# Optimization experiments

Hardware: AMD Instinct MI355X
Metric: run time of the kernel (lower is better)

Reference implementation:

```python
import math
import jax, jax.numpy as jnp
import numpy as np

MUL = 8      # multiplicity of 0e and 1o in irreps_in/out
KS = 5       # kernel spatial extent (diameter 5, steps 1 -> coords -2..2)
NB = 5       # num_radial_basis
RAD = 2.5    # diameter / 2


def _sus(t):
    # e3nn sus(x) = exp(-1/x) for x>0 else 0
    return jnp.where(t > 0.0, jnp.exp(-1.0 / jnp.where(t > 0.0, t, 1.0)), 0.0)


def _emb_sh():
    c = jnp.arange(-2.0, 3.0)
    lat = jnp.stack(jnp.meshgrid(c, c, c, indexing='ij'), axis=-1)  # (5,5,5,3)
    d = jnp.linalg.norm(lat, axis=-1)
    # soft_one_hot_linspace(basis='smooth_finite', cutoff=True)
    values = jnp.linspace(0.0, RAD, NB + 2)
    step = values[1] - values[0]
    diff = (d[..., None] - values[1:-1]) / step
    emb = 1.14136 * math.exp(2.0) * _sus(diff + 1.0) * _sus(1.0 - diff)  # (5,5,5,NB)
    # real spherical harmonics, lmax=2, normalize=True, normalization='component'
    safe = jnp.where(d > 0.0, d, 1.0)[..., None]
    u = jnp.where(d[..., None] > 0.0, lat / safe, 0.0)
    x, y, z = u[..., 0], u[..., 1], u[..., 2]
    s3, s5, s15 = math.sqrt(3.0), math.sqrt(5.0), math.sqrt(15.0)
    sh = jnp.stack([
        jnp.ones_like(x),
        s3 * x, s3 * y, s3 * z,
        s15 * x * z, s15 * x * y,
        s5 * (y * y - 0.5 * (x * x + z * z)),
        s15 * y * z, (s15 / 2.0) * (z * z - x * x),
    ], axis=-1)  # (5,5,5,9)
    return emb, sh


def _c121():
    # Clebsch-Gordan (w3j) for 1o x 2e -> 1o in the real e3nn basis, built from the
    # orthonormal symmetric-traceless matrix basis matching the l=2 SH component order.
    s2, s6 = math.sqrt(2.0), math.sqrt(6.0)
    S = np.zeros((5, 3, 3))
    S[0, 0, 2] = S[0, 2, 0] = 1.0 / s2            # xz
    S[1, 0, 1] = S[1, 1, 0] = 1.0 / s2            # xy
    S[2] = np.diag([-1.0, 2.0, -1.0]) / s6        # 2y^2 - x^2 - z^2
    S[3, 1, 2] = S[3, 2, 1] = 1.0 / s2            # yz
    S[4] = np.diag([-1.0, 0.0, 1.0]) / s2         # z^2 - x^2
    # w3j(1,2,1)[m,j,k] = S[j,m,k]/sqrt(5)  (fully symmetric since l1+l2+l3 even)
    return jnp.asarray(np.transpose(S, (1, 0, 2)) / math.sqrt(5.0), dtype=jnp.float32)


def _build_kernel(weight, emb, sh, c121, dtype):
    g = (KS, KS, KS)
    W = (emb @ weight) / float(KS * KS * KS)  # (5,5,5,320)
    w1, w2, w3, w4, w5 = [W[..., 64 * i:64 * (i + 1)].reshape(g + (MUL, MUL)) for i in range(5)]
    sh0, sh1, sh2 = sh[..., 0], sh[..., 1:4], sh[..., 4:9]
    pw0 = math.sqrt(1.0 / 16.0)   # output 0e: alpha=1, fan_in=8+8
    pw1 = math.sqrt(3.0 / 24.0)   # output 1o: alpha=3, fan_in=8+8+8
    inv_s3 = 1.0 / math.sqrt(3.0)
    K00 = pw0 * sh0[..., None, None] * w1                                   # (g,u,w)
    K01 = (pw1 * inv_s3) * jnp.einsum('xyzuw,xyzk->xyzuwk', w2, sh1)        # (g,u,w,k)
    K10 = (pw0 * inv_s3) * jnp.einsum('xyzuw,xyzm->xyzumw', w4, sh1)        # (g,u,m,w)
    T = jnp.einsum('xyzj,mjk->xyzmk', sh2, c121)                            # (g,m,k)
    eye3 = jnp.eye(3, dtype=dtype)
    K11 = pw1 * (inv_s3 * jnp.einsum('xyzuw,mk->xyzumwk', sh0[..., None, None] * w3, eye3)
                 + jnp.einsum('xyzuw,xyzmk->xyzumwk', w5, T))               # (g,u,m,w,k)
    D = 4 * MUL
    kern = jnp.zeros(g + (D, D), dtype=dtype)
    kern = kern.at[..., :MUL, :MUL].set(K00)
    kern = kern.at[..., :MUL, MUL:].set(K01.reshape(g + (MUL, 3 * MUL)))
    kern = kern.at[..., MUL:, :MUL].set(K10.reshape(g + (3 * MUL, MUL)))
    kern = kern.at[..., MUL:, MUL:].set(K11.reshape(g + (3 * MUL, 3 * MUL)))
    return jnp.transpose(kern, (4, 3, 0, 1, 2))  # 'xyzio->oixyz'


def reference(x, weight, w_sc0, w_sc1):
    emb, sh = _emb_sh()
    c121 = _c121()
    kern = _build_kernel(weight, emb, sh, c121, x.dtype)
    B, _, X, Y, Z = x.shape
    inv_s8 = 1.0 / math.sqrt(MUL)
    # self-connection: e3nn Linear, 0e->0e and 1o->1o blocks
    x0 = x[:, :MUL]
    x1 = x[:, MUL:].reshape(B, MUL, 3, X, Y, Z)
    sc0 = inv_s8 * jnp.einsum('uv,buxyz->bvxyz', w_sc0, x0)
    sc1 = inv_s8 * jnp.einsum('uv,bumxyz->bvmxyz', w_sc1, x1).reshape(B, 3 * MUL, X, Y, Z)
    sc = jnp.concatenate([sc0, sc1], axis=1)
    conv = jax.lax.conv_general_dilated(
        x, kern, window_strides=(1, 1, 1), padding=[(2, 2)] * 3,
        dimension_numbers=('NCDHW', 'OIDHW', 'NCDHW'))
    return sc + conv


def setup_inputs() -> dict:
    key = jax.random.key(0)
    k1, k2, k3, k4 = jax.random.split(key, 4)
    return {
        'x': jax.random.normal(k1, (2, 32, 64, 64, 64), dtype=jnp.float32),
        'weight': jax.random.normal(k2, (NB, 5 * MUL * MUL), dtype=jnp.float32),
        'w_sc0': jax.random.normal(k3, (MUL, MUL), dtype=jnp.float32),
        'w_sc1': jax.random.normal(k4, (MUL, MUL), dtype=jnp.float32),
    }
```

## Files before the change

### kernel.cpp

```cpp
#include <hip/hip_runtime.h>
#include <math.h>

typedef __attribute__((ext_vector_type(8))) short short8;
typedef __attribute__((ext_vector_type(4))) float f32x4;
typedef __attribute__((ext_vector_type(16))) float f32x16;

#define NTAP 125
#define DCH 32

static __device__ __forceinline__ unsigned short f2bf(float f) {
    union { float f; unsigned u; } v; v.f = f;
    unsigned u = v.u;
    return (unsigned short)((u + 0x7FFFu + ((u >> 16) & 1u)) >> 16);
}

static __device__ __forceinline__ void gld_lds16(const void* g, void* l) {
    __builtin_amdgcn_global_load_lds(
        (const __attribute__((address_space(1))) unsigned int*)g,
        (__attribute__((address_space(3))) unsigned int*)l, 16, 0, 0);
}

__global__ __launch_bounds__(128) void build_kern(
    const float* __restrict__ weight,
    const float* __restrict__ w_sc0,
    const float* __restrict__ w_sc1,
    float* __restrict__ kw)
{
    const int t = blockIdx.x;
    const int dx = t / 25, dy = (t / 5) % 5, dz = t % 5;
    const float px = dx - 2.0f, py = dy - 2.0f, pz = dz - 2.0f;
    const float d = sqrtf(px * px + py * py + pz * pz);

    const float stepv = 2.5f / 6.0f;
    const float embc = 1.14136f * expf(2.0f);
    float emb[5];
#pragma unroll
    for (int n = 0; n < 5; ++n) {
        float diff = (d - stepv * (float)(n + 1)) / stepv;
        float a = diff + 1.0f, bb = 1.0f - diff;
        float v = 0.0f;
        if (a > 0.0f && bb > 0.0f)
            v = embc * expf(-1.0f / a) * expf(-1.0f / bb);
        emb[n] = v;
    }

    const float inv_d = (d > 0.0f) ? 1.0f / d : 0.0f;
    const float ux = px * inv_d, uy = py * inv_d, uz = pz * inv_d;
    const float s3 = 1.73205081f, s5 = 2.23606798f, s15 = 3.87298335f;
    float sh[9];
    sh[0] = 1.0f;
    sh[1] = s3 * ux; sh[2] = s3 * uy; sh[3] = s3 * uz;
    sh[4] = s15 * ux * uz;
    sh[5] = s15 * ux * uy;
    sh[6] = s5 * (uy * uy - 0.5f * (ux * ux + uz * uz));
    sh[7] = s15 * uy * uz;
    sh[8] = 0.5f * s15 * (uz * uz - ux * ux);

    const float i_s2 = 0.70710678f, i_s6 = 0.40824829f, i_s5 = 0.44721360f;
    float T[3][3];
    T[0][0] = i_s5 * (-sh[6] * i_s6 - sh[8] * i_s2);
    T[0][1] = i_s5 * (sh[5] * i_s2);
    T[0][2] = i_s5 * (sh[4] * i_s2);
    T[1][0] = T[0][1];
    T[1][1] = i_s5 * (2.0f * sh[6] * i_s6);
    T[1][2] = i_s5 * (sh[7] * i_s2);
    T[2][0] = T[0][2];
    T[2][1] = T[1][2];
    T[2][2] = i_s5 * (-sh[6] * i_s6 + sh[8] * i_s2);

    __shared__ float Wt[320];
    for (int col = threadIdx.x; col < 320; col += 128) {
        float a = 0.0f;
#pragma unroll
        for (int n = 0; n < 5; ++n) a += emb[n] * weight[n * 320 + col];
        Wt[col] = a * (1.0f / 125.0f);
    }
    __syncthreads();

    const float pw0 = 0.25f;
    const float pw1 = 0.35355339f;
    const float inv_s3 = 0.57735027f;
    const float inv_s8 = 0.35355339f;

    for (int idx = threadIdx.x; idx < 1024; idx += 128) {
        const int o = idx >> 5, i = idx & 31;
        float val;
        if (o < 8) {
            if (i < 8) {
                val = pw0 * Wt[i * 8 + o];
            } else {
                const int u = (i - 8) / 3, m = (i - 8) % 3;
                val = pw0 * inv_s3 * Wt[192 + u * 8 + o] * sh[1 + m];
            }
        } else {
            const int v = (o - 8) / 3, k = (o - 8) % 3;
            if (i < 8) {
                val = pw1 * inv_s3 * Wt[64 + i * 8 + v] * sh[1 + k];
            } else {
                const int u = (i - 8) / 3, m = (i - 8) % 3;
                float tv = Wt[256 + u * 8 + v] * T[m][k];
                if (m == k) tv += inv_s3 * Wt[128 + u * 8 + v];
                val = pw1 * tv;
            }
        }
        if (t == 62) {
            if (o < 8 && i < 8) {
                val += inv_s8 * w_sc0[i * 8 + o];
            } else if (o >= 8 && i >= 8) {
                const int u = (i - 8) / 3, m = (i - 8) % 3;
                const int v = (o - 8) / 3, k = (o - 8) % 3;
                if (m == k) val += inv_s8 * w_sc1[u * 8 + v];
            }
        }
        kw[(i * NTAP + t) * DCH + o] = val;
    }
}

__global__ __launch_bounds__(128) void pack_b(
    const float* __restrict__ kw, unsigned short* __restrict__ kwb)
{
    const int t = blockIdx.x;
    const int tid = threadIdx.x;
    const int kh = tid >> 6, l = tid & 63;
    const int co = l & 31;
    const int cib = kh * 16 + (l >> 5) * 8;
    unsigned short v[8];
#pragma unroll
    for (int j = 0; j < 8; ++j)
        v[j] = f2bf(kw[((cib + j) * NTAP + t) * DCH + co]);
    uint4 o;
    o.x = (unsigned)v[0] | ((unsigned)v[1] << 16);
    o.y = (unsigned)v[2] | ((unsigned)v[3] << 16);
    o.z = (unsigned)v[4] | ((unsigned)v[5] << 16);
    o.w = (unsigned)v[6] | ((unsigned)v[7] << 16);
    *reinterpret_cast<uint4*>(kwb + ((size_t)(t * 2 + kh) * 64 + l) * 8) = o;
}

__global__ __launch_bounds__(256) void xpose(
    const float* __restrict__ x, unsigned short* __restrict__ xt)
{
    const int xx = blockIdx.x, yy = blockIdx.y, b = blockIdx.z;
    const int t = threadIdx.x;
    const int z = t & 63, part = t >> 6;
    const float* src = x + ((((size_t)b * 32) * 64 + xx) * 64 + yy) * 64 + z;
    unsigned short v[8];
#pragma unroll
    for (int j = 0; j < 8; ++j)
        v[j] = f2bf(src[(size_t)(part * 8 + j) * 262144]);
    uint4 o;
    o.x = (unsigned)v[0] | ((unsigned)v[1] << 16);
    o.y = (unsigned)v[2] | ((unsigned)v[3] << 16);
    o.z = (unsigned)v[4] | ((unsigned)v[5] << 16);
    o.w = (unsigned)v[6] | ((unsigned)v[7] << 16);
    *reinterpret_cast<uint4*>(
        xt + ((((size_t)b * 64 + xx) * 64 + yy) * 64 + z) * 32 + part * 8) = o;
}

__global__ void zero_fill(float4* p) {
    p[threadIdx.x] = make_float4(0.f, 0.f, 0.f, 0.f);
}

__global__ __launch_bounds__(256, 2) void conv_mfma(
    const unsigned short* __restrict__ xt,
    const unsigned short* __restrict__ kwb,
    const unsigned short* __restrict__ zpage,
    float* __restrict__ out)
{
    extern __shared__ unsigned short smem[];
    char* lds = (char*)smem;

    const int tid = threadIdx.x;
    const int lane = tid & 63;
    const int wv = tid >> 6;
    const int oyp = wv >> 1, zh = wv & 1;
    const int x0 = blockIdx.x * 4, y0 = blockIdx.y * 4;
    const int b = blockIdx.z;
    const int l31 = lane & 31, hi = lane >> 5;

    int abase[5][2];
#pragma unroll
    for (int dz = 0; dz < 5; ++dz) {
        const int s = zh * 32 + l31 + dz;
#pragma unroll
        for (int kh = 0; kh < 2; ++kh) {
            const int cph = (kh * 2 + hi) ^ ((s >> 1) & 3);
            abase[dz][kh] = 51200 + (((((oyp * 2) * 68 + s) << 2) | cph) << 4);
        }
    }
    const int bbase = lane * 16;

    int srow[5]; int soff[5]; bool szok[5];
#pragma unroll
    for (int p = 0; p < 5; ++p) {
        const int c = tid + p * 256;
        const int row = c / 272;
        const int rem = c - row * 272;
        const int slot = rem >> 2;
        const int clog = (rem & 3) ^ ((slot >> 1) & 3);
        const int z = slot - 2;
        srow[p] = row;
        szok[p] = ((unsigned)z < 64u);
        soff[p] = row * 2048 + z * 32 + clog * 8;
    }

    int bsrc[13];
#pragma unroll
    for (int k = 0; k < 13; ++k) {
        const int c = tid + k * 256;
        const int tp = c >> 7, rem = c & 127;
        const int dxx = tp / 5, dzz = tp - dxx * 5;
        bsrc[k] = (dxx * 25 + dzz) * 128 + rem;
    }

    f32x16 acc[2][4];
#pragma unroll
    for (int oyi = 0; oyi < 2; ++oyi)
#pragma unroll
        for (int ox = 0; ox < 4; ++ox)
#pragma unroll
            for (int e = 0; e < 16; ++e) acc[oyi][ox][e] = 0.0f;

    for (int dy = 0; dy < 5; ++dy) {
        const int yyb = y0 + dy - 2;
#pragma unroll
        for (int xl = 0; xl < 8; ++xl) {
            __syncthreads();
            if (xl == 0) {
#pragma unroll
                for (int k = 0; k < 13; ++k) {
                    const int c0 = wv * 64 + k * 256;
                    if (c0 < 3200) {
                        gld_lds16(kwb + ((size_t)(bsrc[k] + dy * 640)) * 8,
                                  lds + c0 * 16);
                    }
                }
            }
            {
                const int xx = x0 + xl - 2;
                const bool xok = ((unsigned)xx < 64u);
                const long long xyb =
                    (long long)(b * 64 + xx) * 131072 + (long long)yyb * 2048;
#pragma unroll
                for (int p = 0; p < 5; ++p) {
                    const int c0 = wv * 64 + p * 256;
                    if (c0 < 1088) {
                        const int yy = yyb + srow[p];
                        const bool ok =
                            xok && ((unsigned)yy < 64u) && szok[p];
                        const unsigned short* src =
                            ok ? (xt + xyb + soff[p]) : zpage;
                        gld_lds16(src, lds + 51200 + c0 * 16);
                    }
                }
            }
            __syncthreads();

#pragma unroll
            for (int dz = 0; dz < 5; ++dz) {
#pragma unroll
                for (int kh = 0; kh < 2; ++kh) {
                    const short8 a0 =
                        *reinterpret_cast<const short8*>(lds + abase[dz][kh]);
                    const short8 a1 = *reinterpret_cast<const short8*>(
                        lds + abase[dz][kh] + 4352);
#pragma unroll
                    for (int ox = 0; ox < 4; ++ox) {
                        const int dxv = xl - ox;
                        if (dxv < 0 || dxv > 4) continue;
                        const short8 bf = *reinterpret_cast<const short8*>(
                            lds + bbase + (((dxv * 5 + dz) * 2 + kh) << 10));
                        acc[0][ox] = __builtin_amdgcn_mfma_f32_32x32x16_bf16(
                            a0, bf, acc[0][ox], 0, 0, 0);
                        acc[1][ox] = __builtin_amdgcn_mfma_f32_32x32x16_bf16(
                            a1, bf, acc[1][ox], 0, 0, 0);
                    }
                }
            }
        }
    }

#pragma unroll
    for (int oyi = 0; oyi < 2; ++oyi) {
        const int yy = y0 + oyp * 2 + oyi;
#pragma unroll
        for (int ox = 0; ox < 4; ++ox) {
            float* base = out +
                ((((size_t)b * 32 + l31) * 64 + (x0 + ox)) * 64 + yy) * 64 +
                zh * 32 + hi * 4;
#pragma unroll
            for (int rq = 0; rq < 4; ++rq) {
                f32x4 v = { acc[oyi][ox][rq * 4 + 0], acc[oyi][ox][rq * 4 + 1],
                            acc[oyi][ox][rq * 4 + 2], acc[oyi][ox][rq * 4 + 3] };
                *reinterpret_cast<f32x4*>(base + rq * 8) = v;
            }
        }
    }
}

extern "C" void kernel_launch(void* const* d_in, const int* in_sizes, int n_in,
                              void* d_out, int out_size, void* d_ws, size_t ws_size,
                              hipStream_t stream) {
    const float* x      = (const float*)d_in[0];
    const float* weight = (const float*)d_in[1];
    const float* w_sc0  = (const float*)d_in[2];
    const float* w_sc1  = (const float*)d_in[3];
    float* out = (float*)d_out;

    char* ws = (char*)d_ws;
    unsigned short* xt  = (unsigned short*)ws;
    float*          kwp = (float*)(ws + 33554432);
    unsigned short* kwb = (unsigned short*)(ws + 34066432);
    unsigned short* zpg = (unsigned short*)(ws + 34322432);

    (void)hipFuncSetAttribute((const void*)conv_mfma,
                              hipFuncAttributeMaxDynamicSharedMemorySize,
                              68608);

    hipLaunchKernelGGL(build_kern, dim3(NTAP), dim3(128), 0, stream,
                       weight, w_sc0, w_sc1, kwp);
    hipLaunchKernelGGL(pack_b, dim3(NTAP), dim3(128), 0, stream, kwp, kwb);
    hipLaunchKernelGGL(xpose, dim3(64, 64, 2), dim3(256), 0, stream, x, xt);
    hipLaunchKernelGGL(zero_fill, dim3(1), dim3(256), 0, stream, (float4*)zpg);
    hipLaunchKernelGGL(conv_mfma, dim3(16, 16, 2), dim3(256), 68608, stream,
                       xt, kwb, zpg, out);
}
```

Baseline: 152.9 us.

## Prefetch next input slab into registers to overlap global loads with MFMA

Input-slab loads move from direct global-to-LDS transfers issued just before use to register prefetches issued one iteration ahead. The data is then written to LDS at the top of the next iteration. Plain __syncthreads is replaced by manual s_waitcnt and s_barrier, with explicit vmcnt counts so the weight loads at xl==0 complete without waiting on the in-flight prefetch. This aims to hide global memory latency behind the MFMA compute. The cost is extra VGPRs, and the hand-counted vmcnt values must stay in step with the number of outstanding loads.

```diff
diff --git a/kernel.cpp b/kernel.cpp
--- a/kernel.cpp
+++ b/kernel.cpp
@@ -212,6 +212,28 @@
         bsrc[k] = (dxx * 25 + dzz) * 128 + rem;
     }
 
+    uint4 R[5];
+    auto issue_slab = [&](int dyn, int xln) {
+        const int yyb = y0 + dyn - 2;
+        const int xx = x0 + xln - 2;
+        const bool xok = ((unsigned)xx < 64u);
+        const long long xyb =
+            (long long)(b * 64 + xx) * 131072 + (long long)yyb * 2048;
+#pragma unroll
+        for (int p = 0; p < 4; ++p) {
+            const int yy = yyb + srow[p];
+            const bool ok = xok && ((unsigned)yy < 64u) && szok[p];
+            const unsigned short* src = ok ? (xt + xyb + soff[p]) : zpage;
+            R[p] = *reinterpret_cast<const uint4*>(src);
+        }
+        if (tid < 64) {
+            const int yy = yyb + srow[4];
+            const bool ok = xok && ((unsigned)yy < 64u) && szok[4];
+            const unsigned short* src = ok ? (xt + xyb + soff[4]) : zpage;
+            R[4] = *reinterpret_cast<const uint4*>(src);
+        }
+    };
+
     f32x16 acc[2][4];
 #pragma unroll
     for (int oyi = 0; oyi < 2; ++oyi)
@@ -220,11 +242,23 @@
 #pragma unroll
             for (int e = 0; e < 16; ++e) acc[oyi][ox][e] = 0.0f;
 
+    issue_slab(0, 0);
+
     for (int dy = 0; dy < 5; ++dy) {
-        const int yyb = y0 + dy - 2;
 #pragma unroll
         for (int xl = 0; xl < 8; ++xl) {
-            __syncthreads();
+            asm volatile("s_waitcnt lgkmcnt(0)" ::: "memory");
+            __builtin_amdgcn_s_barrier();
+            __builtin_amdgcn_sched_barrier(0);
+
+#pragma unroll
+            for (int p = 0; p < 4; ++p)
+                *reinterpret_cast<uint4*>(
+                    lds + 51200 + (tid + p * 256) * 16) = R[p];
+            if (tid < 64)
+                *reinterpret_cast<uint4*>(
+                    lds + 51200 + (tid + 1024) * 16) = R[4];
+
             if (xl == 0) {
 #pragma unroll
                 for (int k = 0; k < 13; ++k) {
@@ -234,26 +268,22 @@
                                   lds + c0 * 16);
                     }
                 }
-            }
-            {
-                const int xx = x0 + xl - 2;
-                const bool xok = ((unsigned)xx < 64u);
-                const long long xyb =
-                    (long long)(b * 64 + xx) * 131072 + (long long)yyb * 2048;
-#pragma unroll
-                for (int p = 0; p < 5; ++p) {
-                    const int c0 = wv * 64 + p * 256;
-                    if (c0 < 1088) {
-                        const int yy = yyb + srow[p];
-                        const bool ok =
-                            xok && ((unsigned)yy < 64u) && szok[p];
-                        const unsigned short* src =
-                            ok ? (xt + xyb + soff[p]) : zpage;
-                        gld_lds16(src, lds + 51200 + c0 * 16);
-                    }
-                }
-            }
-            __syncthreads();
+                __builtin_amdgcn_sched_barrier(0);
+            }
+
+            if (!(dy == 4 && xl == 7)) {
+                issue_slab(xl == 7 ? dy + 1 : dy, xl == 7 ? 0 : xl + 1);
+            }
+
+            asm volatile("s_waitcnt lgkmcnt(0)" ::: "memory");
+            if (xl == 0) {
+                if (wv == 0)
+                    asm volatile("s_waitcnt vmcnt(5)" ::: "memory");
+                else
+                    asm volatile("s_waitcnt vmcnt(4)" ::: "memory");
+            }
+            __builtin_amdgcn_s_barrier();
+            __builtin_amdgcn_sched_barrier(0);
 
 #pragma unroll
             for (int dz = 0; dz < 5; ++dz) {
```

Result: slower. 198.6 us (+29.9%).

## Load activation A fragments directly from global into registers, z-pad transpose buffer

Applied to the files above, without the earlier changes.

The transpose now writes a z-padded layout (68 slots per row, zero halos) so the conv kernel can read A operands straight from global memory into registers instead of staging them through LDS with per-x barriers. Only the weight tile stays in LDS, loaded once per dy, which removes two block syncs per inner step. Blocks grow to 512 threads covering 8 output rows in y, doubling reuse of each LDS weight tile. The cost is that A loads go through L1/L2 with no LDS reuse, so the kernel may become sensitive to global-load latency and register pressure from holding 20 short8 fragments.

```diff
diff --git a/kernel.cpp b/kernel.cpp
--- a/kernel.cpp
+++ b/kernel.cpp
@@ -152,61 +152,47 @@
     o.y = (unsigned)v[2] | ((unsigned)v[3] << 16);
     o.z = (unsigned)v[4] | ((unsigned)v[5] << 16);
     o.w = (unsigned)v[6] | ((unsigned)v[7] << 16);
-    *reinterpret_cast<uint4*>(
-        xt + ((((size_t)b * 64 + xx) * 64 + yy) * 64 + z) * 32 + part * 8) = o;
+    unsigned short* row =
+        xt + (((size_t)b * 64 + xx) * 64 + yy) * 2176;
+    *reinterpret_cast<uint4*>(row + (size_t)(z + 2) * 32 + part * 8) = o;
+    if (t < 16) {
+        const int zi = t >> 2;
+        const int z_idx = (zi < 2) ? zi : 64 + zi;
+        uint4 zz; zz.x = zz.y = zz.z = zz.w = 0u;
+        *reinterpret_cast<uint4*>(row + (size_t)z_idx * 32 + (t & 3) * 8) = zz;
+    }
 }
 
 __global__ void zero_fill(float4* p) {
-    p[threadIdx.x] = make_float4(0.f, 0.f, 0.f, 0.f);
-}
-
-__global__ __launch_bounds__(256, 2) void conv_mfma(
+    float4 z = make_float4(0.f, 0.f, 0.f, 0.f);
+#pragma unroll
+    for (int i = 0; i < 4; ++i) p[threadIdx.x + 256 * i] = z;
+}
+
+__global__ __launch_bounds__(512, 2) void conv_mfma(
     const unsigned short* __restrict__ xt,
     const unsigned short* __restrict__ kwb,
-    const unsigned short* __restrict__ zpage,
+    const unsigned short* __restrict__ zpg,
     float* __restrict__ out)
 {
-    extern __shared__ unsigned short smem[];
-    char* lds = (char*)smem;
+    __shared__ unsigned short Bs[25600];
 
     const int tid = threadIdx.x;
     const int lane = tid & 63;
     const int wv = tid >> 6;
     const int oyp = wv >> 1, zh = wv & 1;
-    const int x0 = blockIdx.x * 4, y0 = blockIdx.y * 4;
+    const int x0 = blockIdx.x * 4, y0 = blockIdx.y * 8;
     const int b = blockIdx.z;
     const int l31 = lane & 31, hi = lane >> 5;
 
-    int abase[5][2];
-#pragma unroll
-    for (int dz = 0; dz < 5; ++dz) {
-        const int s = zh * 32 + l31 + dz;
-#pragma unroll
-        for (int kh = 0; kh < 2; ++kh) {
-            const int cph = (kh * 2 + hi) ^ ((s >> 1) & 3);
-            abase[dz][kh] = 51200 + (((((oyp * 2) * 68 + s) << 2) | cph) << 4);
-        }
-    }
+    const int lanebase = (zh * 32 + l31) * 32 + hi * 8;
+    const char* bsp = (const char*)Bs;
     const int bbase = lane * 16;
 
-    int srow[5]; int soff[5]; bool szok[5];
-#pragma unroll
-    for (int p = 0; p < 5; ++p) {
-        const int c = tid + p * 256;
-        const int row = c / 272;
-        const int rem = c - row * 272;
-        const int slot = rem >> 2;
-        const int clog = (rem & 3) ^ ((slot >> 1) & 3);
-        const int z = slot - 2;
-        srow[p] = row;
-        szok[p] = ((unsigned)z < 64u);
-        soff[p] = row * 2048 + z * 32 + clog * 8;
-    }
-
-    int bsrc[13];
-#pragma unroll
-    for (int k = 0; k < 13; ++k) {
-        const int c = tid + k * 256;
+    int bsrc[7];
+#pragma unroll
+    for (int k = 0; k < 7; ++k) {
+        const int c = tid + k * 512;
         const int tp = c >> 7, rem = c & 127;
         const int dxx = tp / 5, dzz = tp - dxx * 5;
         bsrc[k] = (dxx * 25 + dzz) * 128 + rem;
@@ -221,61 +207,62 @@
             for (int e = 0; e < 16; ++e) acc[oyi][ox][e] = 0.0f;
 
     for (int dy = 0; dy < 5; ++dy) {
-        const int yyb = y0 + dy - 2;
+        __syncthreads();
+#pragma unroll
+        for (int k = 0; k < 7; ++k) {
+            const int c0 = wv * 64 + k * 512;
+            if (c0 < 3200) {
+                gld_lds16(kwb + ((size_t)(bsrc[k] + dy * 640)) * 8,
+                          (char*)Bs + c0 * 16);
+            }
+        }
+        __syncthreads();
+
+        const int yy0 = y0 + oyp * 2 + dy - 2;
+        const bool y0ok = ((unsigned)yy0 < 64u);
+        const bool y1ok = ((unsigned)(yy0 + 1) < 64u);
+
 #pragma unroll
         for (int xl = 0; xl < 8; ++xl) {
-            __syncthreads();
-            if (xl == 0) {
-#pragma unroll
-                for (int k = 0; k < 13; ++k) {
-                    const int c0 = wv * 64 + k * 256;
-                    if (c0 < 3200) {
-                        gld_lds16(kwb + ((size_t)(bsrc[k] + dy * 640)) * 8,
-                                  lds + c0 * 16);
-                    }
+            const int xx = x0 + xl - 2;
+            const bool xok = ((unsigned)xx < 64u);
+
+            const long long sb =
+                ((long long)(b * 64) + xx) * 139264 + lanebase;
+            const unsigned short* p0 = (xok && y0ok)
+                ? xt + sb + (long long)yy0 * 2176 : zpg + lanebase;
+            const unsigned short* p1 = (xok && y1ok)
+                ? xt + sb + (long long)(yy0 + 1) * 2176 : zpg + lanebase;
+
+            short8 A0[5][2], A1[5][2];
+#pragma unroll
+            for (int dz = 0; dz < 5; ++dz)
+#pragma unroll
+                for (int kh = 0; kh < 2; ++kh) {
+                    A0[dz][kh] = *reinterpret_cast<const short8*>(
+                        reinterpret_cast<const char*>(p0) + dz * 64 + kh * 32);
+                    A1[dz][kh] = *reinterpret_cast<const short8*>(
+                        reinterpret_cast<const char*>(p1) + dz * 64 + kh * 32);
                 }
-            }
-            {
-                const int xx = x0 + xl - 2;
-                const bool xok = ((unsigned)xx < 64u);
-                const long long xyb =
-                    (long long)(b * 64 + xx) * 131072 + (long long)yyb * 2048;
-#pragma unroll
-                for (int p = 0; p < 5; ++p) {
-                    const int c0 = wv * 64 + p * 256;
-                    if (c0 < 1088) {
-                        const int yy = yyb + srow[p];
-                        const bool ok =
-                            xok && ((unsigned)yy < 64u) && szok[p];
-                        const unsigned short* src =
-                            ok ? (xt + xyb + soff[p]) : zpage;
-                        gld_lds16(src, lds + 51200 + c0 * 16);
-                    }
-                }
-            }
-            __syncthreads();
-
-#pragma unroll
-            for (int dz = 0; dz < 5; ++dz) {
+
+#pragma unroll
+            for (int dz = 0; dz < 5; ++dz)
 #pragma unroll
                 for (int kh = 0; kh < 2; ++kh) {
-                    const short8 a0 =
-                        *reinterpret_cast<const short8*>(lds + abase[dz][kh]);
-                    const short8 a1 = *reinterpret_cast<const short8*>(
-                        lds + abase[dz][kh] + 4352);
+                    const short8 a0 = A0[dz][kh];
+                    const short8 a1 = A1[dz][kh];
 #pragma unroll
                     for (int ox = 0; ox < 4; ++ox) {
                         const int dxv = xl - ox;
                         if (dxv < 0 || dxv > 4) continue;
                         const short8 bf = *reinterpret_cast<const short8*>(
-                            lds + bbase + (((dxv * 5 + dz) * 2 + kh) << 10));
+                            bsp + bbase + (((dxv * 5 + dz) * 2 + kh) << 10));
                         acc[0][ox] = __builtin_amdgcn_mfma_f32_32x32x16_bf16(
                             a0, bf, acc[0][ox], 0, 0, 0);
                         acc[1][ox] = __builtin_amdgcn_mfma_f32_32x32x16_bf16(
                             a1, bf, acc[1][ox], 0, 0, 0);
                     }
                 }
-            }
         }
     }
 
@@ -308,19 +295,15 @@
 
     char* ws = (char*)d_ws;
     unsigned short* xt  = (unsigned short*)ws;
-    float*          kwp = (float*)(ws + 33554432);
-    unsigned short* kwb = (unsigned short*)(ws + 34066432);
-    unsigned short* zpg = (unsigned short*)(ws + 34322432);
-
-    (void)hipFuncSetAttribute((const void*)conv_mfma,
-                              hipFuncAttributeMaxDynamicSharedMemorySize,
-                              68608);
+    float*          kwp = (float*)(ws + 35651584);
+    unsigned short* kwb = (unsigned short*)(ws + 36163584);
+    unsigned short* zpg = (unsigned short*)(ws + 36419584);
 
     hipLaunchKernelGGL(build_kern, dim3(NTAP), dim3(128), 0, stream,
                        weight, w_sc0, w_sc1, kwp);
     hipLaunchKernelGGL(pack_b, dim3(NTAP), dim3(128), 0, stream, kwp, kwb);
     hipLaunchKernelGGL(xpose, dim3(64, 64, 2), dim3(256), 0, stream, x, xt);
     hipLaunchKernelGGL(zero_fill, dim3(1), dim3(256), 0, stream, (float4*)zpg);
-    hipLaunchKernelGGL(conv_mfma, dim3(16, 16, 2), dim3(256), 68608, stream,
+    hipLaunchKernelGGL(conv_mfma, dim3(16, 8, 2), dim3(512), 0, stream,
                        xt, kwb, zpg, out);
 }
```

Result: slower. 275.2 us (+80.0%).
